# Kernel tuning notes

Hardware: AMD Instinct MI355X
Metric: run time of the kernel (lower is better)

Reference implementation:

```python
import jax, jax.numpy as jnp
import numpy as np

LEFT = 16  # attention window size (previous `left` symbols incl. current)


def _make_history(symbols, left):
    """contexts[b, t, j] = symbols[b, t - (left-1-j)] for j in [0,left),
    padded with symbols[b, 0] for out-of-range positions (pad = symbols[:, :1])."""
    B, T = symbols.shape
    # (T, left) gather index matrix
    idx = jnp.arange(T)[:, None] - (left - 1 - jnp.arange(left))[None, :]
    valid = idx >= 0
    idx_c = jnp.clip(idx, 0, T - 1)
    ctx = symbols[:, idx_c]                                   # (B, T, left)
    pad = symbols[:, :1][:, :, None]                          # (B, 1, 1)
    return jnp.where(valid[None, :, :], ctx, pad)             # (B, T, left)


def setup_inputs() -> dict:
    key = jax.random.key(0)
    k1, k2, k3, k4 = jax.random.split(key, 4)
    B, T, V, D = 8, 2048, 256, 512
    symbols = jax.random.randint(k1, (B, T), 0, V, dtype=jnp.int32)
    encodings = jax.random.normal(k2, (B, T, D), dtype=jnp.float32)
    # keras 'uniform' initializer: U(-0.05, 0.05)
    M = jax.random.uniform(k3, (V, D), minval=-0.05, maxval=0.05, dtype=jnp.float32)
    C = jax.random.uniform(k4, (V, D), minval=-0.05, maxval=0.05, dtype=jnp.float32)
    return {"symbols": symbols, "encodings": encodings, "M": M, "C": C}


def reference(symbols, encodings, M, C):
    contexts = _make_history(symbols, LEFT)                   # (B, T, L) int
    Mg = M[contexts]                                          # (B, T, L, D)
    Cg = C[contexts]                                          # (B, T, L, D)
    scores = jnp.einsum('btld,btd->btl', Mg, encodings)       # (B, T, L)
    p = jax.nn.softmax(scores, axis=-1)                       # (B, T, L)
    compressed = jnp.einsum('btl,btld->btd', p, Cg)           # (B, T, D)
    output = jnp.concatenate([compressed, encodings], axis=-1)  # (B, T, 2D)
    return output, p
```

## Files before the change

kernel.cpp:

```cpp
#include <hip/hip_runtime.h>
#include <hip/hip_bf16.h>

#define B_ 8
#define T_ 2048
#define V_ 256
#define D_ 512
#define LEFT_ 16
#define BT 16
#define NROWS 32

__device__ __forceinline__ float bf_lo(unsigned u) {
    union { unsigned u; float f; } c; c.u = u << 16; return c.f;
}
__device__ __forceinline__ float bf_hi(unsigned u) {
    union { unsigned u; float f; } c; c.u = u & 0xffff0000u; return c.f;
}
__device__ __forceinline__ unsigned pack_bf2(float a, float b) {
    __hip_bfloat162 h = __float22bfloat162_rn(make_float2(a, b));
    union { __hip_bfloat162 h; unsigned u; } c; c.h = h; return c.u;
}

__global__ __launch_bounds__(256, 4)
void attn_cell_kernel(const int* __restrict__ symbols,
                      const float* __restrict__ encodings,
                      const float* __restrict__ M,
                      const float* __restrict__ C,
                      float* __restrict__ out,
                      float* __restrict__ p_out) {
    __shared__ __align__(16) unsigned rows[NROWS][D_ / 2];
    __shared__ __align__(16) float p_s[BT][16];

    const int tid  = threadIdx.x;
    const int lane = tid & 63;
    const int w    = tid >> 6;

    const int blk = blockIdx.x;
    const int b   = blk >> 7;
    const int t0  = (blk & 127) * BT;
    const int* symrow = symbols + b * T_;

    #pragma unroll 4
    for (int i = tid; i < NROWS * (D_ / 4); i += 256) {
        const int r = i >> 7;
        const int c = i & 127;
        int pos = t0 - (LEFT_ - 1) + r;
        pos = max(pos, 0);
        pos = min(pos, T_ - 1);
        const float4 v = reinterpret_cast<const float4*>(M + (size_t)symrow[pos] * D_)[c];
        *reinterpret_cast<uint2*>(&rows[r][c * 2]) =
            make_uint2(pack_bf2(v.x, v.y), pack_bf2(v.z, v.w));
    }
    __syncthreads();

    const int l4 = lane & 15;
    const int rl = ((l4 & 1) << 3) | ((l4 & 2) << 1) | ((l4 & 4) >> 1) | ((l4 & 8) >> 3);

    #pragma unroll
    for (int i = 0; i < 4; ++i) {
        const int lt = w + i * 4;
        const int t  = t0 + lt;
        const size_t ebase = ((size_t)(b * T_ + t)) * D_ + (size_t)lane * 8;
        const float4 e0 = *reinterpret_cast<const float4*>(encodings + ebase);
        const float4 e1 = *reinterpret_cast<const float4*>(encodings + ebase + 4);

        float s[16];
        #pragma unroll
        for (int l = 0; l < 16; ++l) {
            const uint4 m = *reinterpret_cast<const uint4*>(&rows[lt + l][lane * 4]);
            s[l] = bf_lo(m.x) * e0.x + bf_hi(m.x) * e0.y
                 + bf_lo(m.y) * e0.z + bf_hi(m.y) * e0.w
                 + bf_lo(m.z) * e1.x + bf_hi(m.z) * e1.y
                 + bf_lo(m.w) * e1.z + bf_hi(m.w) * e1.w;
        }

        #pragma unroll
        for (int k = 0; k < 8; ++k) {
            const float lo = s[k], hi = s[k + 8];
            const float sd = (lane & 1) ? lo : hi;
            const float rv = __shfl_xor(sd, 1);
            s[k] = (lane & 1) ? hi + rv : lo + rv;
        }
        #pragma unroll
        for (int k = 0; k < 4; ++k) {
            const float lo = s[k], hi = s[k + 4];
            const float sd = (lane & 2) ? lo : hi;
            const float rv = __shfl_xor(sd, 2);
            s[k] = (lane & 2) ? hi + rv : lo + rv;
        }
        #pragma unroll
        for (int k = 0; k < 2; ++k) {
            const float lo = s[k], hi = s[k + 2];
            const float sd = (lane & 4) ? lo : hi;
            const float rv = __shfl_xor(sd, 4);
            s[k] = (lane & 4) ? hi + rv : lo + rv;
        }
        {
            const float lo = s[0], hi = s[1];
            const float sd = (lane & 8) ? lo : hi;
            const float rv = __shfl_xor(sd, 8);
            s[0] = (lane & 8) ? hi + rv : lo + rv;
        }
        float v = s[0];
        v += __shfl_xor(v, 16);
        v += __shfl_xor(v, 32);

        float mx = v;
        mx = fmaxf(mx, __shfl_xor(mx, 1));
        mx = fmaxf(mx, __shfl_xor(mx, 2));
        mx = fmaxf(mx, __shfl_xor(mx, 4));
        mx = fmaxf(mx, __shfl_xor(mx, 8));
        const float e = __expf(v - mx);
        float sum = e;
        sum += __shfl_xor(sum, 1);
        sum += __shfl_xor(sum, 2);
        sum += __shfl_xor(sum, 4);
        sum += __shfl_xor(sum, 8);
        const float p = e / sum;

        if (lane < 16) {
            p_out[((size_t)(b * T_ + t)) * 16 + rl] = p;
            p_s[lt][rl] = p;
        }

        float4* ob = reinterpret_cast<float4*>(out + ((size_t)(b * T_ + t)) * 1024 + D_ + (size_t)lane * 8);
        ob[0] = e0; ob[1] = e1;
    }
    __syncthreads();

    #pragma unroll 4
    for (int i = tid; i < NROWS * (D_ / 4); i += 256) {
        const int r = i >> 7;
        const int c = i & 127;
        int pos = t0 - (LEFT_ - 1) + r;
        pos = max(pos, 0);
        pos = min(pos, T_ - 1);
        const float4 v = reinterpret_cast<const float4*>(C + (size_t)symrow[pos] * D_)[c];
        *reinterpret_cast<uint2*>(&rows[r][c * 2]) =
            make_uint2(pack_bf2(v.x, v.y), pack_bf2(v.z, v.w));
    }
    __syncthreads();

    #pragma unroll
    for (int i = 0; i < 4; ++i) {
        const int lt = w + i * 4;
        const int t  = t0 + lt;
        const float4 q0 = *reinterpret_cast<const float4*>(&p_s[lt][0]);
        const float4 q1 = *reinterpret_cast<const float4*>(&p_s[lt][4]);
        const float4 q2 = *reinterpret_cast<const float4*>(&p_s[lt][8]);
        const float4 q3 = *reinterpret_cast<const float4*>(&p_s[lt][12]);
        const float pw[16] = { q0.x, q0.y, q0.z, q0.w, q1.x, q1.y, q1.z, q1.w,
                               q2.x, q2.y, q2.z, q2.w, q3.x, q3.y, q3.z, q3.w };

        float4 a0 = make_float4(0.f, 0.f, 0.f, 0.f);
        float4 a1 = make_float4(0.f, 0.f, 0.f, 0.f);
        #pragma unroll
        for (int l = 0; l < 16; ++l) {
            const uint4 c4 = *reinterpret_cast<const uint4*>(&rows[lt + l][lane * 4]);
            const float pl = pw[l];
            a0.x += pl * bf_lo(c4.x); a0.y += pl * bf_hi(c4.x);
            a0.z += pl * bf_lo(c4.y); a0.w += pl * bf_hi(c4.y);
            a1.x += pl * bf_lo(c4.z); a1.y += pl * bf_hi(c4.z);
            a1.z += pl * bf_lo(c4.w); a1.w += pl * bf_hi(c4.w);
        }
        float4* ob = reinterpret_cast<float4*>(out + ((size_t)(b * T_ + t)) * 1024 + (size_t)lane * 8);
        ob[0] = a0; ob[1] = a1;
    }
}

extern "C" void kernel_launch(void* const* d_in, const int* in_sizes, int n_in,
                              void* d_out, int out_size, void* d_ws, size_t ws_size,
                              hipStream_t stream) {
    const int*   symbols   = (const int*)d_in[0];
    const float* encodings = (const float*)d_in[1];
    const float* M         = (const float*)d_in[2];
    const float* C         = (const float*)d_in[3];
    float* out   = (float*)d_out;
    float* p_out = out + (size_t)B_ * T_ * 1024;

    dim3 grid(B_ * (T_ / BT));
    attn_cell_kernel<<<grid, 256, 0, stream>>>(symbols, encodings, M, C, out, p_out);
}
```

Measured before the change: 36.14 us.

## Compute scores and weighted sum with bf16 MFMA instructions over swizzled LDS tiles

Replaces the per-lane scalar dot products and shuffle reductions with MFMA 16x16x32 bf16 instructions. M rows are stored in an XOR-swizzled layout for the score MFMA, and partial sums are reduced across waves through LDS. C is stored transposed so a banded probability matrix can be multiplied by MFMA. This cuts VALU and shuffle work, but adds strided scalar LDS stores for the transpose, an extra barrier, and lowers the occupancy hint from 4 to 3.

```diff
diff --git a/kernel.cpp b/kernel.cpp
--- a/kernel.cpp
+++ b/kernel.cpp
@@ -9,101 +9,121 @@
 #define BT 16
 #define NROWS 32
 
-__device__ __forceinline__ float bf_lo(unsigned u) {
-    union { unsigned u; float f; } c; c.u = u << 16; return c.f;
-}
-__device__ __forceinline__ float bf_hi(unsigned u) {
-    union { unsigned u; float f; } c; c.u = u & 0xffff0000u; return c.f;
-}
+typedef short bf16x8 __attribute__((ext_vector_type(8)));
+typedef float f32x4 __attribute__((ext_vector_type(4)));
+typedef unsigned long long u64;
+
+union FragU { unsigned u[4]; u64 ull[2]; bf16x8 v; };
+
 __device__ __forceinline__ unsigned pack_bf2(float a, float b) {
     __hip_bfloat162 h = __float22bfloat162_rn(make_float2(a, b));
     union { __hip_bfloat162 h; unsigned u; } c; c.h = h; return c.u;
 }
-
-__global__ __launch_bounds__(256, 4)
+__device__ __forceinline__ unsigned short bf1(float x) {
+    union { __hip_bfloat16 h; unsigned short s; } c; c.h = __float2bfloat16(x); return c.s;
+}
+
+#define SMEM_BYTES 42496
+#define SPART_OFF 32768
+#define PLDS_OFF  41472
+
+__global__ __launch_bounds__(256, 3)
 void attn_cell_kernel(const int* __restrict__ symbols,
                       const float* __restrict__ encodings,
                       const float* __restrict__ M,
                       const float* __restrict__ C,
                       float* __restrict__ out,
                       float* __restrict__ p_out) {
-    __shared__ __align__(16) unsigned rows[NROWS][D_ / 2];
-    __shared__ __align__(16) float p_s[BT][16];
+    __shared__ __align__(16) char smem[SMEM_BYTES];
 
     const int tid  = threadIdx.x;
     const int lane = tid & 63;
     const int w    = tid >> 6;
+    const int q    = lane >> 4;
+    const int t16  = lane & 15;
 
     const int blk = blockIdx.x;
     const int b   = blk >> 7;
     const int t0  = (blk & 127) * BT;
     const int* symrow = symbols + b * T_;
-
-    #pragma unroll 4
-    for (int i = tid; i < NROWS * (D_ / 4); i += 256) {
-        const int r = i >> 7;
-        const int c = i & 127;
-        int pos = t0 - (LEFT_ - 1) + r;
-        pos = max(pos, 0);
-        pos = min(pos, T_ - 1);
-        const float4 v = reinterpret_cast<const float4*>(M + (size_t)symrow[pos] * D_)[c];
-        *reinterpret_cast<uint2*>(&rows[r][c * 2]) =
-            make_uint2(pack_bf2(v.x, v.y), pack_bf2(v.z, v.w));
-    }
-    __syncthreads();
-
-    const int l4 = lane & 15;
-    const int rl = ((l4 & 1) << 3) | ((l4 & 2) << 1) | ((l4 & 4) >> 1) | ((l4 & 8) >> 3);
-
-    #pragma unroll
-    for (int i = 0; i < 4; ++i) {
-        const int lt = w + i * 4;
-        const int t  = t0 + lt;
-        const size_t ebase = ((size_t)(b * T_ + t)) * D_ + (size_t)lane * 8;
-        const float4 e0 = *reinterpret_cast<const float4*>(encodings + ebase);
-        const float4 e1 = *reinterpret_cast<const float4*>(encodings + ebase + 4);
-
-        float s[16];
-        #pragma unroll
-        for (int l = 0; l < 16; ++l) {
-            const uint4 m = *reinterpret_cast<const uint4*>(&rows[lt + l][lane * 4]);
-            s[l] = bf_lo(m.x) * e0.x + bf_hi(m.x) * e0.y
-                 + bf_lo(m.y) * e0.z + bf_hi(m.y) * e0.w
-                 + bf_lo(m.z) * e1.x + bf_hi(m.z) * e1.y
-                 + bf_lo(m.w) * e1.z + bf_hi(m.w) * e1.w;
-        }
-
-        #pragma unroll
-        for (int k = 0; k < 8; ++k) {
-            const float lo = s[k], hi = s[k + 8];
-            const float sd = (lane & 1) ? lo : hi;
-            const float rv = __shfl_xor(sd, 1);
-            s[k] = (lane & 1) ? hi + rv : lo + rv;
-        }
-        #pragma unroll
-        for (int k = 0; k < 4; ++k) {
-            const float lo = s[k], hi = s[k + 4];
-            const float sd = (lane & 2) ? lo : hi;
-            const float rv = __shfl_xor(sd, 2);
-            s[k] = (lane & 2) ? hi + rv : lo + rv;
-        }
-        #pragma unroll
-        for (int k = 0; k < 2; ++k) {
-            const float lo = s[k], hi = s[k + 2];
-            const float sd = (lane & 4) ? lo : hi;
-            const float rv = __shfl_xor(sd, 4);
-            s[k] = (lane & 4) ? hi + rv : lo + rv;
-        }
-        {
-            const float lo = s[0], hi = s[1];
-            const float sd = (lane & 8) ? lo : hi;
-            const float rv = __shfl_xor(sd, 8);
-            s[0] = (lane & 8) ? hi + rv : lo + rv;
-        }
-        float v = s[0];
-        v += __shfl_xor(v, 16);
-        v += __shfl_xor(v, 32);
-
+    const size_t rowbase = (size_t)(b * T_ + t0);
+
+    ((unsigned*)(smem + PLDS_OFF))[tid] = 0u;
+
+    {
+        u64* r8 = (u64*)smem;
+        #pragma unroll 2
+        for (int i = tid; i < 2048; i += 256) {
+            const int j = i >> 6;
+            const int g = i & 63;
+            int pos = t0 - (LEFT_ - 1) + j;
+            pos = max(pos, 0); pos = min(pos, T_ - 1);
+            const float* src = M + (size_t)symrow[pos] * D_ + g * 8;
+            const float4 v0 = ((const float4*)src)[0];
+            const float4 v1 = ((const float4*)src)[1];
+            const u64 lo = (u64)pack_bf2(v0.x, v0.y) | ((u64)pack_bf2(v0.z, v0.w) << 32);
+            const u64 hi = (u64)pack_bf2(v1.x, v1.y) | ((u64)pack_bf2(v1.z, v1.w) << 32);
+            const int c = j & 7;
+            r8[j * 128 + ((2 * g) ^ c)]     = lo;
+            r8[j * 128 + ((2 * g + 1) ^ c)] = hi;
+        }
+    }
+    __syncthreads();
+
+    {
+        float4 lo[4], hi[4];
+        const float* ebase = encodings + (rowbase + t16) * D_;
+        float* obase = out + (rowbase + t16) * 1024 + D_;
+        #pragma unroll
+        for (int ks = 0; ks < 4; ++ks) {
+            const int d0 = 128 * w + 32 * ks + 4 * q;
+            lo[ks] = *(const float4*)(ebase + d0);
+            hi[ks] = *(const float4*)(ebase + d0 + 16);
+        }
+        bf16x8 bfrag[4];
+        #pragma unroll
+        for (int ks = 0; ks < 4; ++ks) {
+            const int d0 = 128 * w + 32 * ks + 4 * q;
+            *(float4*)(obase + d0)      = lo[ks];
+            *(float4*)(obase + d0 + 16) = hi[ks];
+            FragU u;
+            u.u[0] = pack_bf2(lo[ks].x, lo[ks].y);
+            u.u[1] = pack_bf2(lo[ks].z, lo[ks].w);
+            u.u[2] = pack_bf2(hi[ks].x, hi[ks].y);
+            u.u[3] = pack_bf2(hi[ks].z, hi[ks].w);
+            bfrag[ks] = u.v;
+        }
+        const u64* r8 = (const u64*)smem;
+        f32x4 acc0 = {0.f, 0.f, 0.f, 0.f}, acc1 = {0.f, 0.f, 0.f, 0.f};
+        const int j0 = t16, j1 = t16 + 16;
+        const int c0 = j0 & 7, c1 = j1 & 7;
+        #pragma unroll
+        for (int ks = 0; ks < 4; ++ks) {
+            const int gb = 32 * w + 8 * ks + q;
+            FragU a0, a1;
+            a0.ull[0] = r8[j0 * 128 + ((gb)     ^ c0)];
+            a0.ull[1] = r8[j0 * 128 + ((gb + 4) ^ c0)];
+            a1.ull[0] = r8[j1 * 128 + ((gb)     ^ c1)];
+            a1.ull[1] = r8[j1 * 128 + ((gb + 4) ^ c1)];
+            acc0 = __builtin_amdgcn_mfma_f32_16x16x32_bf16(a0.v, bfrag[ks], acc0, 0, 0, 0);
+            acc1 = __builtin_amdgcn_mfma_f32_16x16x32_bf16(a1.v, bfrag[ks], acc1, 0, 0, 0);
+        }
+        float* spart = (float*)(smem + SPART_OFF);
+        #pragma unroll
+        for (int r = 0; r < 4; ++r) {
+            spart[(w * 32 + 4 * q + r) * 17 + t16]      = acc0[r];
+            spart[(w * 32 + 16 + 4 * q + r) * 17 + t16] = acc1[r];
+        }
+    }
+    __syncthreads();
+
+    {
+        const int l = t16;
+        const int t = 4 * w + q;
+        const int j = t + l;
+        const float* spart = (const float*)(smem + SPART_OFF);
+        float v = spart[j * 17 + t] + spart[(32 + j) * 17 + t]
+                + spart[(64 + j) * 17 + t] + spart[(96 + j) * 17 + t];
         float mx = v;
         mx = fmaxf(mx, __shfl_xor(mx, 1));
         mx = fmaxf(mx, __shfl_xor(mx, 2));
@@ -116,54 +136,53 @@
         sum += __shfl_xor(sum, 4);
         sum += __shfl_xor(sum, 8);
         const float p = e / sum;
-
-        if (lane < 16) {
-            p_out[((size_t)(b * T_ + t)) * 16 + rl] = p;
-            p_s[lt][rl] = p;
-        }
-
-        float4* ob = reinterpret_cast<float4*>(out + ((size_t)(b * T_ + t)) * 1024 + D_ + (size_t)lane * 8);
-        ob[0] = e0; ob[1] = e1;
-    }
-    __syncthreads();
-
-    #pragma unroll 4
-    for (int i = tid; i < NROWS * (D_ / 4); i += 256) {
-        const int r = i >> 7;
-        const int c = i & 127;
-        int pos = t0 - (LEFT_ - 1) + r;
-        pos = max(pos, 0);
-        pos = min(pos, T_ - 1);
-        const float4 v = reinterpret_cast<const float4*>(C + (size_t)symrow[pos] * D_)[c];
-        *reinterpret_cast<uint2*>(&rows[r][c * 2]) =
-            make_uint2(pack_bf2(v.x, v.y), pack_bf2(v.z, v.w));
-    }
-    __syncthreads();
-
-    #pragma unroll
-    for (int i = 0; i < 4; ++i) {
-        const int lt = w + i * 4;
-        const int t  = t0 + lt;
-        const float4 q0 = *reinterpret_cast<const float4*>(&p_s[lt][0]);
-        const float4 q1 = *reinterpret_cast<const float4*>(&p_s[lt][4]);
-        const float4 q2 = *reinterpret_cast<const float4*>(&p_s[lt][8]);
-        const float4 q3 = *reinterpret_cast<const float4*>(&p_s[lt][12]);
-        const float pw[16] = { q0.x, q0.y, q0.z, q0.w, q1.x, q1.y, q1.z, q1.w,
-                               q2.x, q2.y, q2.z, q2.w, q3.x, q3.y, q3.z, q3.w };
-
-        float4 a0 = make_float4(0.f, 0.f, 0.f, 0.f);
-        float4 a1 = make_float4(0.f, 0.f, 0.f, 0.f);
-        #pragma unroll
-        for (int l = 0; l < 16; ++l) {
-            const uint4 c4 = *reinterpret_cast<const uint4*>(&rows[lt + l][lane * 4]);
-            const float pl = pw[l];
-            a0.x += pl * bf_lo(c4.x); a0.y += pl * bf_hi(c4.x);
-            a0.z += pl * bf_lo(c4.y); a0.w += pl * bf_hi(c4.y);
-            a1.x += pl * bf_lo(c4.z); a1.y += pl * bf_hi(c4.z);
-            a1.z += pl * bf_lo(c4.w); a1.w += pl * bf_hi(c4.w);
-        }
-        float4* ob = reinterpret_cast<float4*>(out + ((size_t)(b * T_ + t)) * 1024 + (size_t)lane * 8);
-        ob[0] = a0; ob[1] = a1;
+        p_out[(rowbase + t) * 16 + l] = p;
+        ((unsigned short*)(smem + PLDS_OFF))[t * 32 + j] = bf1(p);
+    }
+    __syncthreads();
+
+    {
+        unsigned short* ct = (unsigned short*)smem;
+        #pragma unroll 2
+        for (int i = tid; i < 2048; i += 256) {
+            const int j = i & 31;
+            const int g = i >> 5;
+            int pos = t0 - (LEFT_ - 1) + j;
+            pos = max(pos, 0); pos = min(pos, T_ - 1);
+            const float* src = C + (size_t)symrow[pos] * D_ + g * 8;
+            const float4 v0 = ((const float4*)src)[0];
+            const float4 v1 = ((const float4*)src)[1];
+            const int dbase = g * 8;
+            ct[(dbase + 0) * 40 + j] = bf1(v0.x);
+            ct[(dbase + 1) * 40 + j] = bf1(v0.y);
+            ct[(dbase + 2) * 40 + j] = bf1(v0.z);
+            ct[(dbase + 3) * 40 + j] = bf1(v0.w);
+            ct[(dbase + 4) * 40 + j] = bf1(v1.x);
+            ct[(dbase + 5) * 40 + j] = bf1(v1.y);
+            ct[(dbase + 6) * 40 + j] = bf1(v1.z);
+            ct[(dbase + 7) * 40 + j] = bf1(v1.w);
+        }
+    }
+    __syncthreads();
+
+    {
+        const u64* p8 = (const u64*)(smem + PLDS_OFF);
+        FragU ap;
+        ap.ull[0] = p8[t16 * 8 + q];
+        ap.ull[1] = p8[t16 * 8 + q + 4];
+        const u64* ct8 = (const u64*)smem;
+        #pragma unroll
+        for (int m = 0; m < 8; ++m) {
+            const int d = (w * 8 + m) * 16 + t16;
+            FragU bc;
+            bc.ull[0] = ct8[d * 10 + q];
+            bc.ull[1] = ct8[d * 10 + q + 4];
+            f32x4 acc = {0.f, 0.f, 0.f, 0.f};
+            acc = __builtin_amdgcn_mfma_f32_16x16x32_bf16(ap.v, bc.v, acc, 0, 0, 0);
+            #pragma unroll
+            for (int r = 0; r < 4; ++r)
+                out[(rowbase + 4 * q + r) * 1024 + d] = acc[r];
+        }
     }
 }
 
```

New measurement: 35.29 us. 1.02x faster.

## Replace shared-memory bf16 staging with per-wave register-blocked fp32 gathers

Applied to the files above, without the earlier changes.

Removes the shared-memory staging of M and C rows, along with the bf16 conversion and the block barriers. Each wave now handles 4 consecutive timesteps and reads the 19 needed M and C rows straight from global memory (L2-resident tables), reusing each row across the 4 timesteps in registers. All 64 scores per wave are reduced with one multi-value butterfly shuffle transpose, and p is broadcast by shuffles for the weighted sum. This keeps fp32 precision, but raises register pressure (64 score accumulators plus 8 float4 accumulators) and costs more redundant global row loads than the block-wide 32-row shared tile did.

```diff
diff --git a/kernel.cpp b/kernel.cpp
--- a/kernel.cpp
+++ b/kernel.cpp
@@ -1,169 +1,170 @@
 #include <hip/hip_runtime.h>
-#include <hip/hip_bf16.h>
 
 #define B_ 8
 #define T_ 2048
 #define V_ 256
 #define D_ 512
 #define LEFT_ 16
-#define BT 16
-#define NROWS 32
+#define TPW 4
+#define NR (TPW + LEFT_ - 1)
 
-__device__ __forceinline__ float bf_lo(unsigned u) {
-    union { unsigned u; float f; } c; c.u = u << 16; return c.f;
-}
-__device__ __forceinline__ float bf_hi(unsigned u) {
-    union { unsigned u; float f; } c; c.u = u & 0xffff0000u; return c.f;
-}
-__device__ __forceinline__ unsigned pack_bf2(float a, float b) {
-    __hip_bfloat162 h = __float22bfloat162_rn(make_float2(a, b));
-    union { __hip_bfloat162 h; unsigned u; } c; c.h = h; return c.u;
+__device__ __forceinline__ constexpr int rev6(int x) {
+    return (((x >> 0) & 1) << 5) | (((x >> 1) & 1) << 4) | (((x >> 2) & 1) << 3) |
+           (((x >> 3) & 1) << 2) | (((x >> 4) & 1) << 1) | (((x >> 5) & 1) << 0);
 }
 
-__global__ __launch_bounds__(256, 4)
+__device__ __forceinline__ float dot8(const float4& m0, const float4& m1,
+                                      const float4& e0, const float4& e1) {
+    return m0.x * e0.x + m0.y * e0.y + m0.z * e0.z + m0.w * e0.w
+         + m1.x * e1.x + m1.y * e1.y + m1.z * e1.z + m1.w * e1.w;
+}
+
+__global__ __launch_bounds__(256)
 void attn_cell_kernel(const int* __restrict__ symbols,
                       const float* __restrict__ encodings,
                       const float* __restrict__ M,
                       const float* __restrict__ C,
                       float* __restrict__ out,
                       float* __restrict__ p_out) {
-    __shared__ __align__(16) unsigned rows[NROWS][D_ / 2];
-    __shared__ __align__(16) float p_s[BT][16];
-
     const int tid  = threadIdx.x;
     const int lane = tid & 63;
     const int w    = tid >> 6;
 
     const int blk = blockIdx.x;
     const int b   = blk >> 7;
-    const int t0  = (blk & 127) * BT;
+    const int tb  = (blk & 127) * 16 + w * TPW;
     const int* symrow = symbols + b * T_;
+    const size_t rowbase = (size_t)b * T_ + tb;
+    const int dof = lane * 8;
 
-    #pragma unroll 4
-    for (int i = tid; i < NROWS * (D_ / 4); i += 256) {
-        const int r = i >> 7;
-        const int c = i & 127;
-        int pos = t0 - (LEFT_ - 1) + r;
+    int syms[NR];
+    #pragma unroll
+    for (int i = 0; i < NR; ++i) {
+        int pos = tb - (LEFT_ - 1) + i;
         pos = max(pos, 0);
-        pos = min(pos, T_ - 1);
-        const float4 v = reinterpret_cast<const float4*>(M + (size_t)symrow[pos] * D_)[c];
-        *reinterpret_cast<uint2*>(&rows[r][c * 2]) =
-            make_uint2(pack_bf2(v.x, v.y), pack_bf2(v.z, v.w));
+        syms[i] = symrow[pos];
     }
-    __syncthreads();
 
-    const int l4 = lane & 15;
-    const int rl = ((l4 & 1) << 3) | ((l4 & 2) << 1) | ((l4 & 4) >> 1) | ((l4 & 8) >> 3);
+    float4 e0[TPW], e1[TPW];
+    #pragma unroll
+    for (int tk = 0; tk < TPW; ++tk) {
+        const float* e = encodings + (rowbase + tk) * D_ + dof;
+        e0[tk] = *(const float4*)e;
+        e1[tk] = *(const float4*)(e + 4);
+    }
+
+    float s[64];
+    #pragma unroll
+    for (int v = 0; v < 64; ++v) s[v] = 0.f;
 
     #pragma unroll
-    for (int i = 0; i < 4; ++i) {
-        const int lt = w + i * 4;
-        const int t  = t0 + lt;
-        const size_t ebase = ((size_t)(b * T_ + t)) * D_ + (size_t)lane * 8;
-        const float4 e0 = *reinterpret_cast<const float4*>(encodings + ebase);
-        const float4 e1 = *reinterpret_cast<const float4*>(encodings + ebase + 4);
-
-        float s[16];
+    for (int i = 0; i < NR; ++i) {
+        const float* mr = M + (size_t)syms[i] * D_ + dof;
+        const float4 m0 = *(const float4*)mr;
+        const float4 m1 = *(const float4*)(mr + 4);
         #pragma unroll
-        for (int l = 0; l < 16; ++l) {
-            const uint4 m = *reinterpret_cast<const uint4*>(&rows[lt + l][lane * 4]);
-            s[l] = bf_lo(m.x) * e0.x + bf_hi(m.x) * e0.y
-                 + bf_lo(m.y) * e0.z + bf_hi(m.y) * e0.w
-                 + bf_lo(m.z) * e1.x + bf_hi(m.z) * e1.y
-                 + bf_lo(m.w) * e1.z + bf_hi(m.w) * e1.w;
+        for (int tk = 0; tk < TPW; ++tk) {
+            const int sl = i - tk;
+            if (sl >= 0 && sl < 16)
+                s[(tk << 4) | sl] += dot8(m0, m1, e0[tk], e1[tk]);
         }
-
-        #pragma unroll
-        for (int k = 0; k < 8; ++k) {
-            const float lo = s[k], hi = s[k + 8];
-            const float sd = (lane & 1) ? lo : hi;
-            const float rv = __shfl_xor(sd, 1);
-            s[k] = (lane & 1) ? hi + rv : lo + rv;
-        }
-        #pragma unroll
-        for (int k = 0; k < 4; ++k) {
-            const float lo = s[k], hi = s[k + 4];
-            const float sd = (lane & 2) ? lo : hi;
-            const float rv = __shfl_xor(sd, 2);
-            s[k] = (lane & 2) ? hi + rv : lo + rv;
-        }
-        #pragma unroll
-        for (int k = 0; k < 2; ++k) {
-            const float lo = s[k], hi = s[k + 2];
-            const float sd = (lane & 4) ? lo : hi;
-            const float rv = __shfl_xor(sd, 4);
-            s[k] = (lane & 4) ? hi + rv : lo + rv;
-        }
-        {
-            const float lo = s[0], hi = s[1];
-            const float sd = (lane & 8) ? lo : hi;
-            const float rv = __shfl_xor(sd, 8);
-            s[0] = (lane & 8) ? hi + rv : lo + rv;
-        }
-        float v = s[0];
-        v += __shfl_xor(v, 16);
-        v += __shfl_xor(v, 32);
-
-        float mx = v;
-        mx = fmaxf(mx, __shfl_xor(mx, 1));
-        mx = fmaxf(mx, __shfl_xor(mx, 2));
-        mx = fmaxf(mx, __shfl_xor(mx, 4));
-        mx = fmaxf(mx, __shfl_xor(mx, 8));
-        const float e = __expf(v - mx);
-        float sum = e;
-        sum += __shfl_xor(sum, 1);
-        sum += __shfl_xor(sum, 2);
-        sum += __shfl_xor(sum, 4);
-        sum += __shfl_xor(sum, 8);
-        const float p = e / sum;
-
-        if (lane < 16) {
-            p_out[((size_t)(b * T_ + t)) * 16 + rl] = p;
-            p_s[lt][rl] = p;
-        }
-
-        float4* ob = reinterpret_cast<float4*>(out + ((size_t)(b * T_ + t)) * 1024 + D_ + (size_t)lane * 8);
-        ob[0] = e0; ob[1] = e1;
     }
-    __syncthreads();
-
-    #pragma unroll 4
-    for (int i = tid; i < NROWS * (D_ / 4); i += 256) {
-        const int r = i >> 7;
-        const int c = i & 127;
-        int pos = t0 - (LEFT_ - 1) + r;
-        pos = max(pos, 0);
-        pos = min(pos, T_ - 1);
-        const float4 v = reinterpret_cast<const float4*>(C + (size_t)symrow[pos] * D_)[c];
-        *reinterpret_cast<uint2*>(&rows[r][c * 2]) =
-            make_uint2(pack_bf2(v.x, v.y), pack_bf2(v.z, v.w));
-    }
-    __syncthreads();
 
     #pragma unroll
-    for (int i = 0; i < 4; ++i) {
-        const int lt = w + i * 4;
-        const int t  = t0 + lt;
-        const float4 q0 = *reinterpret_cast<const float4*>(&p_s[lt][0]);
-        const float4 q1 = *reinterpret_cast<const float4*>(&p_s[lt][4]);
-        const float4 q2 = *reinterpret_cast<const float4*>(&p_s[lt][8]);
-        const float4 q3 = *reinterpret_cast<const float4*>(&p_s[lt][12]);
-        const float pw[16] = { q0.x, q0.y, q0.z, q0.w, q1.x, q1.y, q1.z, q1.w,
-                               q2.x, q2.y, q2.z, q2.w, q3.x, q3.y, q3.z, q3.w };
+    for (int k = 0; k < 32; ++k) {
+        const float lo = s[k], hi = s[k + 32];
+        const float sd = (lane & 1) ? lo : hi;
+        const float rv = __shfl_xor(sd, 1);
+        s[k] = (lane & 1) ? hi + rv : lo + rv;
+    }
+    #pragma unroll
+    for (int k = 0; k < 16; ++k) {
+        const float lo = s[k], hi = s[k + 16];
+        const float sd = (lane & 2) ? lo : hi;
+        const float rv = __shfl_xor(sd, 2);
+        s[k] = (lane & 2) ? hi + rv : lo + rv;
+    }
+    #pragma unroll
+    for (int k = 0; k < 8; ++k) {
+        const float lo = s[k], hi = s[k + 8];
+        const float sd = (lane & 4) ? lo : hi;
+        const float rv = __shfl_xor(sd, 4);
+        s[k] = (lane & 4) ? hi + rv : lo + rv;
+    }
+    #pragma unroll
+    for (int k = 0; k < 4; ++k) {
+        const float lo = s[k], hi = s[k + 4];
+        const float sd = (lane & 8) ? lo : hi;
+        const float rv = __shfl_xor(sd, 8);
+        s[k] = (lane & 8) ? hi + rv : lo + rv;
+    }
+    #pragma unroll
+    for (int k = 0; k < 2; ++k) {
+        const float lo = s[k], hi = s[k + 2];
+        const float sd = (lane & 16) ? lo : hi;
+        const float rv = __shfl_xor(sd, 16);
+        s[k] = (lane & 16) ? hi + rv : lo + rv;
+    }
+    {
+        const float lo = s[0], hi = s[1];
+        const float sd = (lane & 32) ? lo : hi;
+        const float rv = __shfl_xor(sd, 32);
+        s[0] = (lane & 32) ? hi + rv : lo + rv;
+    }
+    const float v = s[0];
 
-        float4 a0 = make_float4(0.f, 0.f, 0.f, 0.f);
-        float4 a1 = make_float4(0.f, 0.f, 0.f, 0.f);
+    float mx = v;
+    mx = fmaxf(mx, __shfl_xor(mx, 4));
+    mx = fmaxf(mx, __shfl_xor(mx, 8));
+    mx = fmaxf(mx, __shfl_xor(mx, 16));
+    mx = fmaxf(mx, __shfl_xor(mx, 32));
+    const float ex = __expf(v - mx);
+    float sum = ex;
+    sum += __shfl_xor(sum, 4);
+    sum += __shfl_xor(sum, 8);
+    sum += __shfl_xor(sum, 16);
+    sum += __shfl_xor(sum, 32);
+    const float p = ex / sum;
+
+    {
+        const int idx  = rev6(lane);
+        const int tk_o = idx >> 4;
+        const int sl_o = idx & 15;
+        p_out[(rowbase + tk_o) * 16 + sl_o] = p;
+    }
+
+    float4 a0[TPW], a1[TPW];
+    #pragma unroll
+    for (int tk = 0; tk < TPW; ++tk) {
+        a0[tk] = make_float4(0.f, 0.f, 0.f, 0.f);
+        a1[tk] = make_float4(0.f, 0.f, 0.f, 0.f);
+    }
+
+    #pragma unroll
+    for (int i = 0; i < NR; ++i) {
+        const float* cr = C + (size_t)syms[i] * D_ + dof;
+        const float4 c0 = *(const float4*)cr;
+        const float4 c1 = *(const float4*)(cr + 4);
         #pragma unroll
-        for (int l = 0; l < 16; ++l) {
-            const uint4 c4 = *reinterpret_cast<const uint4*>(&rows[lt + l][lane * 4]);
-            const float pl = pw[l];
-            a0.x += pl * bf_lo(c4.x); a0.y += pl * bf_hi(c4.x);
-            a0.z += pl * bf_lo(c4.y); a0.w += pl * bf_hi(c4.y);
-            a1.x += pl * bf_lo(c4.z); a1.y += pl * bf_hi(c4.z);
-            a1.z += pl * bf_lo(c4.w); a1.w += pl * bf_hi(c4.w);
+        for (int tk = 0; tk < TPW; ++tk) {
+            const int sl = i - tk;
+            if (sl >= 0 && sl < 16) {
+                const float pb = __shfl(p, rev6((tk << 4) | sl));
+                a0[tk].x += pb * c0.x; a0[tk].y += pb * c0.y;
+                a0[tk].z += pb * c0.z; a0[tk].w += pb * c0.w;
+                a1[tk].x += pb * c1.x; a1[tk].y += pb * c1.y;
+                a1[tk].z += pb * c1.z; a1[tk].w += pb * c1.w;
+            }
         }
-        float4* ob = reinterpret_cast<float4*>(out + ((size_t)(b * T_ + t)) * 1024 + (size_t)lane * 8);
-        ob[0] = a0; ob[1] = a1;
+    }
+
+    #pragma unroll
+    for (int tk = 0; tk < TPW; ++tk) {
+        float* ob = out + (rowbase + tk) * 1024 + dof;
+        *(float4*)ob       = a0[tk];
+        *(float4*)(ob + 4) = a1[tk];
+        *(float4*)(ob + D_)     = e0[tk];
+        *(float4*)(ob + D_ + 4) = e1[tk];
     }
 }
 
@@ -177,6 +178,6 @@
     float* out   = (float*)d_out;
     float* p_out = out + (size_t)B_ * T_ * 1024;
 
-    dim3 grid(B_ * (T_ / BT));
+    dim3 grid(B_ * (T_ / 16));
     attn_cell_kernel<<<grid, 256, 0, stream>>>(symbols, encodings, M, C, out, p_out);
 }
```

New measurement: 33.30 us. 7.9% less time.
